# Optimization experiments

Measured on AMD Instinct MI355X. Metric: run time of the kernel, lower is better.

The kernel has to match this reference:

```python
import jax, jax.numpy as jnp
import numpy as np
import math

N_NODES = 50000
N_EDGES = 800000
HIDDEN = 128
NUM_GAUSS = 50
NUM_FILTERS = 128
CUTOFF = 10.0
SHIFT = math.log(2.0)


def setup_inputs() -> dict:
    key = jax.random.key(0)
    ks = jax.random.split(key, 12)
    x = jax.random.normal(ks[0], (N_NODES, HIDDEN), dtype=jnp.float32)
    edge_index = jax.random.randint(ks[1], (2, N_EDGES), 0, N_NODES, dtype=jnp.int64)
    edge_weight = jax.random.uniform(ks[2], (N_EDGES,), dtype=jnp.float32)
    edge_attr = jax.random.normal(ks[3], (N_EDGES, NUM_GAUSS), dtype=jnp.float32)
    # learned parameters (xavier-ish scale)
    def xavier(k, shape):
        fan_in, fan_out = shape[1], shape[0]
        bound = math.sqrt(6.0 / (fan_in + fan_out))
        return jax.random.uniform(k, shape, dtype=jnp.float32, minval=-bound, maxval=bound)
    mlp_w1 = xavier(ks[4], (NUM_FILTERS, NUM_GAUSS))
    mlp_b1 = jnp.zeros((NUM_FILTERS,), jnp.float32)
    mlp_w2 = xavier(ks[5], (NUM_FILTERS, NUM_FILTERS))
    mlp_b2 = jnp.zeros((NUM_FILTERS,), jnp.float32)
    lin1_w = xavier(ks[6], (NUM_FILTERS, HIDDEN))   # no bias
    lin2_w = xavier(ks[7], (HIDDEN, NUM_FILTERS))
    lin2_b = jnp.zeros((HIDDEN,), jnp.float32)
    lin_w = xavier(ks[8], (HIDDEN, HIDDEN))
    lin_b = jnp.zeros((HIDDEN,), jnp.float32)
    return {"x": x, "edge_index": edge_index, "edge_weight": edge_weight,
            "edge_attr": edge_attr, "mlp_w1": mlp_w1, "mlp_b1": mlp_b1,
            "mlp_w2": mlp_w2, "mlp_b2": mlp_b2, "lin1_w": lin1_w,
            "lin2_w": lin2_w, "lin2_b": lin2_b, "lin_w": lin_w, "lin_b": lin_b}


def shifted_softplus(v):
    return jax.nn.softplus(v) - SHIFT


def reference(x, edge_index, edge_weight, edge_attr, mlp_w1, mlp_b1,
              mlp_w2, mlp_b2, lin1_w, lin2_w, lin2_b, lin_w, lin_b):
    src, dst = edge_index[0], edge_index[1]
    # cosine cutoff per edge: [E]
    C = 0.5 * (jnp.cos(edge_weight * (jnp.pi / CUTOFF)) + 1.0)
    # edge filter MLP: [E, num_filters]
    h_e = shifted_softplus(edge_attr @ mlp_w1.T + mlp_b1)
    W = (h_e @ mlp_w2.T + mlp_b2) * C[:, None]
    # node projection, gather-multiply-scatter aggregation
    h = x @ lin1_w.T                       # [N, num_filters]
    msg = h[src] * W                       # [E, num_filters]
    agg = jax.ops.segment_sum(msg, dst, num_segments=N_NODES)  # [N, num_filters]
    h = agg @ lin2_w.T + lin2_b            # [N, hidden]
    h = shifted_softplus(h)
    out = h @ lin_w.T + lin_b              # [N, hidden]
    return out
```

## Files before the change

kernel.cpp:

```cpp
#include <hip/hip_runtime.h>
#include <hip/hip_bf16.h>
#include <math.h>

#define E_NUM 800000
#define NN 50000
#define NG 50
#define NTW (E_NUM / 16)
#define EDGE_BLOCKS 768

typedef __bf16 bf16x8 __attribute__((ext_vector_type(8)));
typedef float f32x4 __attribute__((ext_vector_type(4)));
typedef unsigned short ushortx8 __attribute__((ext_vector_type(8)));

__device__ __forceinline__ unsigned short f2b(float f) {
  union { float f; unsigned u; } v; v.f = f;
  unsigned u = v.u;
  u += 0x7fffu + ((u >> 16) & 1u);
  return (unsigned short)(u >> 16);
}
__device__ __forceinline__ float b2f(unsigned short u) {
  union { unsigned u; float f; } v; v.u = ((unsigned)u) << 16; return v.f;
}
__device__ __forceinline__ float sspf(float v) {
  float e = __builtin_amdgcn_exp2f(-1.4426950408889634f * fabsf(v));
  return fmaxf(v, 0.f) + 0.6931471805599453f * __builtin_amdgcn_logf(fmaf(0.5f, e, 0.5f));
}

__global__ __launch_bounds__(256) void k_hist(const int* __restrict__ ei, int* __restrict__ counts) {
  int e = blockIdx.x * 256 + threadIdx.x;
  if (e < E_NUM) atomicAdd(&counts[ei[E_NUM + e]], 1);
}

__global__ __launch_bounds__(1024) void k_scan(const int* __restrict__ counts,
                                               int* __restrict__ cursor, int* __restrict__ off) {
  __shared__ int tot[1024];
  const int t = threadIdx.x;
  const int C = (NN + 1023) >> 10;
  int lo = t * C, hi = lo + C; if (hi > NN) hi = NN; if (lo > NN) lo = NN;
  int s = 0;
  for (int i = lo; i < hi; ++i) s += counts[i];
  tot[t] = s;
  __syncthreads();
  int mine = s;
  for (int o = 1; o < 1024; o <<= 1) {
    int v = (t >= o) ? tot[t - o] : 0;
    __syncthreads();
    tot[t] += v;
    __syncthreads();
  }
  int run = tot[t] - mine;
  for (int i = lo; i < hi; ++i) { int c = counts[i]; cursor[i] = run; off[i] = run; run += c; }
  if (t == 1023) off[NN] = E_NUM;
}

__global__ __launch_bounds__(256) void k_scatter2(const int* __restrict__ ei,
                                                  int* __restrict__ cursor, int* __restrict__ inv,
                                                  int* __restrict__ srcS) {
  int e = blockIdx.x * 256 + threadIdx.x;
  if (e < E_NUM) {
    int d = ei[E_NUM + e];
    int pos = atomicAdd(&cursor[d], 1);
    inv[e] = pos;
    srcS[pos] = ei[e];
  }
}

__global__ __launch_bounds__(256) void k_mfma_gemm(
    const float* __restrict__ X, const float* __restrict__ Wm,
    const float* __restrict__ bias, float* __restrict__ out, int act, int nrows)
{
  __shared__ __attribute__((aligned(16))) unsigned short s_x[128 * 128];
  __shared__ __attribute__((aligned(16))) unsigned short s_w[128 * 128];
  const int tid = threadIdx.x;
  const int w = tid >> 6, lane = tid & 63, q = lane >> 4, n16 = lane & 15;
  const int base = blockIdx.x * 128;

  for (int c = tid; c < 128 * 16; c += 256) {
    int f = c >> 4, ch = c & 15;
    const float4* wp = (const float4*)(Wm + f * 128 + ch * 8);
    float4 v0 = wp[0], v1 = wp[1];
    ushortx8 v = { f2b(v0.x), f2b(v0.y), f2b(v0.z), f2b(v0.w),
                   f2b(v1.x), f2b(v1.y), f2b(v1.z), f2b(v1.w) };
    *(ushortx8*)&s_w[(f << 7) + ((ch ^ (f & 15)) << 3)] = v;
  }
  for (int c = tid; c < 128 * 16; c += 256) {
    int r = c >> 4, ch = c & 15;
    int n = base + r;
    float4 v0 = {0.f, 0.f, 0.f, 0.f}, v1 = v0;
    if (n < nrows) {
      const float4* xp = (const float4*)(X + (long)n * 128 + ch * 8);
      v0 = xp[0]; v1 = xp[1];
    }
    ushortx8 v = { f2b(v0.x), f2b(v0.y), f2b(v0.z), f2b(v0.w),
                   f2b(v1.x), f2b(v1.y), f2b(v1.z), f2b(v1.w) };
    *(ushortx8*)&s_x[(r << 7) + ((ch ^ (r & 15)) << 3)] = v;
  }
  __syncthreads();

  float bv[8];
#pragma unroll
  for (int t = 0; t < 8; ++t) bv[t] = bias ? bias[t * 16 + n16] : 0.f;

  bf16x8 a[2][4];
#pragma unroll
  for (int g = 0; g < 2; ++g) {
    int r = w * 32 + g * 16 + n16;
#pragma unroll
    for (int ks = 0; ks < 4; ++ks)
      a[g][ks] = *(const bf16x8*)&s_x[(r << 7) + (((ks * 4 + q) ^ (r & 15)) << 3)];
  }
#pragma unroll
  for (int t = 0; t < 8; ++t) {
    int f = t * 16 + n16;
    bf16x8 b[4];
#pragma unroll
    for (int ks = 0; ks < 4; ++ks)
      b[ks] = *(const bf16x8*)&s_w[(f << 7) + (((ks * 4 + q) ^ (f & 15)) << 3)];
#pragma unroll
    for (int g = 0; g < 2; ++g) {
      f32x4 acc = {0.f, 0.f, 0.f, 0.f};
#pragma unroll
      for (int ks = 0; ks < 4; ++ks)
        acc = __builtin_amdgcn_mfma_f32_16x16x32_bf16(a[g][ks], b[ks], acc, 0, 0, 0);
#pragma unroll
      for (int r = 0; r < 4; ++r) {
        int n = base + w * 32 + g * 16 + q * 4 + r;
        if (n < nrows) {
          float v = acc[r] + bv[t];
          if (act) v = sspf(v);
          out[(long)n * 128 + f] = v;
        }
      }
    }
  }
}

__global__ __launch_bounds__(256, 3) void k_edge2(
    const float* __restrict__ attr, const int* __restrict__ ei,
    const float* __restrict__ ew, const float* __restrict__ w1,
    const float* __restrict__ b1, const float* __restrict__ w2,
    const float* __restrict__ b2, const float* __restrict__ h,
    const int* __restrict__ inv, float* __restrict__ agg,
    unsigned short* __restrict__ Wsrt, int mode)
{
  __shared__ __attribute__((aligned(16))) unsigned short s_w2[128 * 128];
  __shared__ __attribute__((aligned(16))) unsigned short s_scr[4 * 16 * 136];

  const int tid  = threadIdx.x;
  const int w    = tid >> 6;
  const int lane = tid & 63;
  const int q    = lane >> 4;
  const int n16  = lane & 15;

  for (int i = tid; i < 128 * 128; i += 256) {
    int f = i >> 7, k = i & 127;
    int pos = (f << 7) + ((((k >> 3) ^ (f & 15)) << 3)) + (k & 7);
    s_w2[pos] = f2b(w2[i]);
  }
  bf16x8 w1A[8], w1B[8];
#pragma unroll
  for (int t = 0; t < 8; ++t) {
    int f = t * 16 + n16;
    const float* row = w1 + f * NG;
    union { ushortx8 u; bf16x8 b; } ua, ub;
#pragma unroll
    for (int j = 0; j < 8; ++j) ua.u[j] = f2b(row[q * 8 + j]);
#pragma unroll
    for (int j = 0; j < 8; ++j) { int k = 32 + q * 8 + j; ub.u[j] = (k < NG) ? f2b(row[k]) : (unsigned short)0; }
    w1A[t] = ua.b; w1B[t] = ub.b;
  }
  float b1v[8], b2v[8];
#pragma unroll
  for (int t = 0; t < 8; ++t) {
    b1v[t] = b1[t * 16 + n16];
    b2v[t] = b2[t * 16 + n16];
  }
  __syncthreads();

  unsigned short* scr = s_scr + w * (16 * 136);
  const int nwaves = EDGE_BLOCKS * 4;
  const int gw = blockIdx.x * 4 + w;

  for (int tile = gw; tile < NTW; tile += nwaves) {
    const int e0 = tile * 16;
    const int er = e0 + n16;
    const float* rp = attr + (long)er * NG;

    float2 p0 = *(const float2*)(rp + q * 8);
    float2 p1 = *(const float2*)(rp + q * 8 + 2);
    float2 p2 = *(const float2*)(rp + q * 8 + 4);
    float2 p3 = *(const float2*)(rp + q * 8 + 6);
    float2 p4 = {0.f, 0.f}, p5 = {0.f, 0.f}, p6 = {0.f, 0.f}, p7 = {0.f, 0.f};
    if (q < 2) {
      const float* rp2 = rp + 32 + q * 8;
      p4 = *(const float2*)(rp2);
      p5 = *(const float2*)(rp2 + 2);
      p6 = *(const float2*)(rp2 + 4);
      p7 = *(const float2*)(rp2 + 6);
    } else if (q == 2) {
      p4 = *(const float2*)(rp + 48);
    }
    union { ushortx8 u; bf16x8 b; } ua, ub;
    ua.u[0] = f2b(p0.x); ua.u[1] = f2b(p0.y); ua.u[2] = f2b(p1.x); ua.u[3] = f2b(p1.y);
    ua.u[4] = f2b(p2.x); ua.u[5] = f2b(p2.y); ua.u[6] = f2b(p3.x); ua.u[7] = f2b(p3.y);
    ub.u[0] = f2b(p4.x); ub.u[1] = f2b(p4.y); ub.u[2] = f2b(p5.x); ub.u[3] = f2b(p5.y);
    ub.u[4] = f2b(p6.x); ub.u[5] = f2b(p6.y); ub.u[6] = f2b(p7.x); ub.u[7] = f2b(p7.y);

#pragma unroll
    for (int t = 0; t < 8; ++t) {
      f32x4 acc = {0.f, 0.f, 0.f, 0.f};
      acc = __builtin_amdgcn_mfma_f32_16x16x32_bf16(ua.b, w1A[t], acc, 0, 0, 0);
      acc = __builtin_amdgcn_mfma_f32_16x16x32_bf16(ub.b, w1B[t], acc, 0, 0, 0);
      int f = t * 16 + n16;
#pragma unroll
      for (int r = 0; r < 4; ++r) {
        int row = q * 4 + r;
        scr[row * 136 + f] = f2b(sspf(acc[r] + b1v[t]));
      }
    }
    __builtin_amdgcn_wave_barrier();

    bf16x8 a2f[4];
#pragma unroll
    for (int ks = 0; ks < 4; ++ks)
      a2f[ks] = *(const bf16x8*)&scr[n16 * 136 + ks * 32 + q * 8];
    __builtin_amdgcn_wave_barrier();

    float cvv[4];
#pragma unroll
    for (int r = 0; r < 4; ++r)
      cvv[r] = 0.5f * (__builtin_amdgcn_cosf(ew[e0 + q * 4 + r] * 0.05f) + 1.f);

    int srcv[4], dstv[4];
    if (mode == 0) {
#pragma unroll
      for (int r = 0; r < 4; ++r) {
        srcv[r] = ei[e0 + q * 4 + r];
        dstv[r] = ei[E_NUM + e0 + q * 4 + r];
      }
    }

#pragma unroll
    for (int t = 0; t < 8; ++t) {
      int f = t * 16 + n16;
      f32x4 acc = {0.f, 0.f, 0.f, 0.f};
#pragma unroll
      for (int ks = 0; ks < 4; ++ks) {
        bf16x8 bb = *(const bf16x8*)&s_w2[(f << 7) + (((ks * 4 + q) ^ (f & 15)) << 3)];
        acc = __builtin_amdgcn_mfma_f32_16x16x32_bf16(a2f[ks], bb, acc, 0, 0, 0);
      }
      if (mode == 1) {
#pragma unroll
        for (int r = 0; r < 4; ++r) {
          int row = q * 4 + r;
          scr[row * 136 + f] = f2b((acc[r] + b2v[t]) * cvv[r]);
        }
      } else {
#pragma unroll
        for (int r = 0; r < 4; ++r) {
          float msg = h[(long)srcv[r] * 128 + f] * (acc[r] + b2v[t]) * cvv[r];
          atomicAdd(&agg[(long)dstv[r] * 128 + f], msg);
        }
      }
    }

    if (mode == 1) {
      __builtin_amdgcn_wave_barrier();
#pragma unroll
      for (int i = 0; i < 4; ++i) {
        int row = i * 4 + q;
        int pos = inv[e0 + row];
        ushortx8 v = *(const ushortx8*)&scr[row * 136 + n16 * 8];
        __builtin_nontemporal_store(v, (ushortx8*)(Wsrt + (long)pos * 128 + n16 * 8));
      }
      __builtin_amdgcn_wave_barrier();
    }
  }
}

__global__ __launch_bounds__(256) void k_e2(
    const unsigned short* __restrict__ Wsrt, const int* __restrict__ srcS,
    const int* __restrict__ off, const float* __restrict__ h, float* __restrict__ agg)
{
  const int wv = threadIdx.x >> 6, lane = threadIdx.x & 63;
  const int n = blockIdx.x * 4 + wv;
  const int j0 = off[n], j1 = off[n + 1];
  float ax = 0.f, ay = 0.f;
  int j = j0;
  for (; j + 4 <= j1; j += 4) {
    int s0 = srcS[j], s1 = srcS[j + 1], s2 = srcS[j + 2], s3 = srcS[j + 3];
    unsigned w0 = __builtin_nontemporal_load((const unsigned*)(Wsrt + (long)(j    ) * 128) + lane);
    unsigned w1_ = __builtin_nontemporal_load((const unsigned*)(Wsrt + (long)(j + 1) * 128) + lane);
    unsigned w2_ = __builtin_nontemporal_load((const unsigned*)(Wsrt + (long)(j + 2) * 128) + lane);
    unsigned w3_ = __builtin_nontemporal_load((const unsigned*)(Wsrt + (long)(j + 3) * 128) + lane);
    float2 h0 = *(const float2*)(h + (long)s0 * 128 + lane * 2);
    float2 h1 = *(const float2*)(h + (long)s1 * 128 + lane * 2);
    float2 h2 = *(const float2*)(h + (long)s2 * 128 + lane * 2);
    float2 h3 = *(const float2*)(h + (long)s3 * 128 + lane * 2);
    ax += h0.x * b2f((unsigned short)(w0 & 0xffffu)) + h1.x * b2f((unsigned short)(w1_ & 0xffffu))
        + h2.x * b2f((unsigned short)(w2_ & 0xffffu)) + h3.x * b2f((unsigned short)(w3_ & 0xffffu));
    ay += h0.y * b2f((unsigned short)(w0 >> 16)) + h1.y * b2f((unsigned short)(w1_ >> 16))
        + h2.y * b2f((unsigned short)(w2_ >> 16)) + h3.y * b2f((unsigned short)(w3_ >> 16));
  }
  for (; j < j1; ++j) {
    int s = srcS[j];
    unsigned wp = __builtin_nontemporal_load((const unsigned*)(Wsrt + (long)j * 128) + lane);
    float2 hp = *(const float2*)(h + (long)s * 128 + lane * 2);
    ax += hp.x * b2f((unsigned short)(wp & 0xffffu));
    ay += hp.y * b2f((unsigned short)(wp >> 16));
  }
  float2 o; o.x = ax; o.y = ay;
  *(float2*)(agg + (long)n * 128 + lane * 2) = o;
}

extern "C" void kernel_launch(void* const* d_in, const int* in_sizes, int n_in,
                              void* d_out, int out_size, void* d_ws, size_t ws_size,
                              hipStream_t stream) {
  const float* x     = (const float*)d_in[0];
  const int*   ei    = (const int*)  d_in[1];
  const float* ew    = (const float*)d_in[2];
  const float* attr  = (const float*)d_in[3];
  const float* w1    = (const float*)d_in[4];
  const float* b1    = (const float*)d_in[5];
  const float* w2    = (const float*)d_in[6];
  const float* b2    = (const float*)d_in[7];
  const float* lin1w = (const float*)d_in[8];
  const float* lin2w = (const float*)d_in[9];
  const float* lin2b = (const float*)d_in[10];
  const float* linw  = (const float*)d_in[11];
  const float* linb  = (const float*)d_in[12];
  float* out = (float*)d_out;

  char* base = (char*)d_ws;
  float* agg    = (float*)base;
  float* h      = agg + (size_t)NN * 128;
  int*   counts = (int*)(h + (size_t)NN * 128);
  int*   cursor = counts + NN;
  int*   off    = cursor + NN;
  int*   inv    = off + NN + 1;
  int*   srcS   = inv + E_NUM;
  size_t head   = (size_t)((char*)(srcS + E_NUM) - base);
  size_t woff   = (head + 255) & ~(size_t)255;
  unsigned short* Wsrt = (unsigned short*)(base + woff);
  size_t need = woff + (size_t)E_NUM * 128 * sizeof(unsigned short);
  const int mode = (ws_size >= need) ? 1 : 0;

  const int gemm_grid = (NN + 127) / 128;
  if (mode == 1) {
    (void)hipMemsetAsync(counts, 0, (size_t)NN * sizeof(int), stream);
    k_hist<<<(E_NUM + 255) / 256, 256, 0, stream>>>(ei, counts);
    k_scan<<<1, 1024, 0, stream>>>(counts, cursor, off);
    k_scatter2<<<(E_NUM + 255) / 256, 256, 0, stream>>>(ei, cursor, inv, srcS);
    k_edge2<<<EDGE_BLOCKS, 256, 0, stream>>>(attr, ei, ew, w1, b1, w2, b2, h, inv, agg, Wsrt, 1);
    k_mfma_gemm<<<gemm_grid, 256, 0, stream>>>(x, lin1w, nullptr, h, 0, NN);
    k_e2<<<NN / 4, 256, 0, stream>>>(Wsrt, srcS, off, h, agg);
  } else {
    (void)hipMemsetAsync(agg, 0, (size_t)NN * 128 * sizeof(float), stream);
    k_mfma_gemm<<<gemm_grid, 256, 0, stream>>>(x, lin1w, nullptr, h, 0, NN);
    k_edge2<<<EDGE_BLOCKS, 256, 0, stream>>>(attr, ei, ew, w1, b1, w2, b2, h, inv, agg, Wsrt, 0);
  }
  k_mfma_gemm<<<gemm_grid, 256, 0, stream>>>(agg, lin2w, lin2b, h, 1, NN);
  k_mfma_gemm<<<gemm_grid, 256, 0, stream>>>(h, linw, linb, out, 0, NN);
}
```

Baseline: 672.4 us.

## Fuse edge filter with sorted-segment aggregation and fuse the two output GEMMs

The edge kernel now processes edges in dst-sorted order. It gathers attr and edge_weight through a permutation, then reduces each 16-edge tile's messages per destination in registers. Interior runs are plain stores and boundary runs use atomics, so the bf16 W buffer and the separate k_e2 aggregation pass are gone. The last two node GEMMs are fused into one kernel that keeps the intermediate in shared memory. This removes the large write and read of the per-edge filter matrix, but adds scattered attr gathers, atomics at tile boundaries and a full agg memset.

```diff
diff --git a/kernel.cpp b/kernel.cpp
--- a/kernel.cpp
+++ b/kernel.cpp
@@ -13,10 +13,7 @@
 typedef unsigned short ushortx8 __attribute__((ext_vector_type(8)));
 
 __device__ __forceinline__ unsigned short f2b(float f) {
-  union { float f; unsigned u; } v; v.f = f;
-  unsigned u = v.u;
-  u += 0x7fffu + ((u >> 16) & 1u);
-  return (unsigned short)(u >> 16);
+  union { __bf16 h; unsigned short u; } v; v.h = (__bf16)f; return v.u;
 }
 __device__ __forceinline__ float b2f(unsigned short u) {
   union { unsigned u; float f; } v; v.u = ((unsigned)u) << 16; return v.f;
@@ -54,14 +51,16 @@
 }
 
 __global__ __launch_bounds__(256) void k_scatter2(const int* __restrict__ ei,
-                                                  int* __restrict__ cursor, int* __restrict__ inv,
-                                                  int* __restrict__ srcS) {
+                                                  int* __restrict__ cursor,
+                                                  int* __restrict__ srcS, int* __restrict__ dstS,
+                                                  int* __restrict__ eS) {
   int e = blockIdx.x * 256 + threadIdx.x;
   if (e < E_NUM) {
     int d = ei[E_NUM + e];
     int pos = atomicAdd(&cursor[d], 1);
-    inv[e] = pos;
     srcS[pos] = ei[e];
+    dstS[pos] = d;
+    eS[pos] = e;
   }
 }
 
@@ -135,13 +134,129 @@
   }
 }
 
-__global__ __launch_bounds__(256, 3) void k_edge2(
+__global__ __launch_bounds__(256, 2) void k_gemm23(
+    const float* __restrict__ A, const float* __restrict__ W2,
+    const float* __restrict__ B2, const float* __restrict__ W3,
+    const float* __restrict__ B3, float* __restrict__ out, int nrows)
+{
+  __shared__ __attribute__((aligned(16))) unsigned short s_x[128 * 128];
+  __shared__ __attribute__((aligned(16))) unsigned short s_w[128 * 128];
+  const int tid = threadIdx.x;
+  const int w = tid >> 6, lane = tid & 63, q = lane >> 4, n16 = lane & 15;
+  const int base = blockIdx.x * 128;
+
+  for (int c = tid; c < 128 * 16; c += 256) {
+    int f = c >> 4, ch = c & 15;
+    const float4* wp = (const float4*)(W2 + f * 128 + ch * 8);
+    float4 v0 = wp[0], v1 = wp[1];
+    ushortx8 v = { f2b(v0.x), f2b(v0.y), f2b(v0.z), f2b(v0.w),
+                   f2b(v1.x), f2b(v1.y), f2b(v1.z), f2b(v1.w) };
+    *(ushortx8*)&s_w[(f << 7) + ((ch ^ (f & 15)) << 3)] = v;
+  }
+  for (int c = tid; c < 128 * 16; c += 256) {
+    int r = c >> 4, ch = c & 15;
+    int n = base + r;
+    float4 v0 = {0.f, 0.f, 0.f, 0.f}, v1 = v0;
+    if (n < nrows) {
+      const float4* xp = (const float4*)(A + (long)n * 128 + ch * 8);
+      v0 = xp[0]; v1 = xp[1];
+    }
+    ushortx8 v = { f2b(v0.x), f2b(v0.y), f2b(v0.z), f2b(v0.w),
+                   f2b(v1.x), f2b(v1.y), f2b(v1.z), f2b(v1.w) };
+    *(ushortx8*)&s_x[(r << 7) + ((ch ^ (r & 15)) << 3)] = v;
+  }
+  __syncthreads();
+
+  float b2v[8], b3v[8];
+#pragma unroll
+  for (int t = 0; t < 8; ++t) { b2v[t] = B2[t * 16 + n16]; b3v[t] = B3[t * 16 + n16]; }
+
+  bf16x8 a[2][4];
+#pragma unroll
+  for (int g = 0; g < 2; ++g) {
+    int r = w * 32 + g * 16 + n16;
+#pragma unroll
+    for (int ks = 0; ks < 4; ++ks)
+      a[g][ks] = *(const bf16x8*)&s_x[(r << 7) + (((ks * 4 + q) ^ (r & 15)) << 3)];
+  }
+  float acc1[8][2][4];
+#pragma unroll
+  for (int t = 0; t < 8; ++t) {
+    int f = t * 16 + n16;
+    bf16x8 b[4];
+#pragma unroll
+    for (int ks = 0; ks < 4; ++ks)
+      b[ks] = *(const bf16x8*)&s_w[(f << 7) + (((ks * 4 + q) ^ (f & 15)) << 3)];
+#pragma unroll
+    for (int g = 0; g < 2; ++g) {
+      f32x4 acc = {0.f, 0.f, 0.f, 0.f};
+#pragma unroll
+      for (int ks = 0; ks < 4; ++ks)
+        acc = __builtin_amdgcn_mfma_f32_16x16x32_bf16(a[g][ks], b[ks], acc, 0, 0, 0);
+#pragma unroll
+      for (int r = 0; r < 4; ++r) acc1[t][g][r] = acc[r];
+    }
+  }
+  __syncthreads();
+
+#pragma unroll
+  for (int t = 0; t < 8; ++t) {
+    int f = t * 16 + n16;
+#pragma unroll
+    for (int g = 0; g < 2; ++g)
+#pragma unroll
+      for (int r = 0; r < 4; ++r) {
+        int row = w * 32 + g * 16 + q * 4 + r;
+        s_x[(row << 7) + (((f >> 3) ^ (row & 15)) << 3) + (f & 7)] =
+            f2b(sspf(acc1[t][g][r] + b2v[t]));
+      }
+  }
+  for (int c = tid; c < 128 * 16; c += 256) {
+    int f = c >> 4, ch = c & 15;
+    const float4* wp = (const float4*)(W3 + f * 128 + ch * 8);
+    float4 v0 = wp[0], v1 = wp[1];
+    ushortx8 v = { f2b(v0.x), f2b(v0.y), f2b(v0.z), f2b(v0.w),
+                   f2b(v1.x), f2b(v1.y), f2b(v1.z), f2b(v1.w) };
+    *(ushortx8*)&s_w[(f << 7) + ((ch ^ (f & 15)) << 3)] = v;
+  }
+  __syncthreads();
+
+#pragma unroll
+  for (int g = 0; g < 2; ++g) {
+    int r = w * 32 + g * 16 + n16;
+#pragma unroll
+    for (int ks = 0; ks < 4; ++ks)
+      a[g][ks] = *(const bf16x8*)&s_x[(r << 7) + (((ks * 4 + q) ^ (r & 15)) << 3)];
+  }
+#pragma unroll
+  for (int t = 0; t < 8; ++t) {
+    int f = t * 16 + n16;
+    bf16x8 b[4];
+#pragma unroll
+    for (int ks = 0; ks < 4; ++ks)
+      b[ks] = *(const bf16x8*)&s_w[(f << 7) + (((ks * 4 + q) ^ (f & 15)) << 3)];
+#pragma unroll
+    for (int g = 0; g < 2; ++g) {
+      f32x4 acc = {0.f, 0.f, 0.f, 0.f};
+#pragma unroll
+      for (int ks = 0; ks < 4; ++ks)
+        acc = __builtin_amdgcn_mfma_f32_16x16x32_bf16(a[g][ks], b[ks], acc, 0, 0, 0);
+#pragma unroll
+      for (int r = 0; r < 4; ++r) {
+        int n = base + w * 32 + g * 16 + q * 4 + r;
+        if (n < nrows) out[(long)n * 128 + f] = acc[r] + b3v[t];
+      }
+    }
+  }
+}
+
+__global__ __launch_bounds__(256, 3) void k_edge_agg(
     const float* __restrict__ attr, const int* __restrict__ ei,
     const float* __restrict__ ew, const float* __restrict__ w1,
     const float* __restrict__ b1, const float* __restrict__ w2,
     const float* __restrict__ b2, const float* __restrict__ h,
-    const int* __restrict__ inv, float* __restrict__ agg,
-    unsigned short* __restrict__ Wsrt, int mode)
+    const int* __restrict__ srcS, const int* __restrict__ dstS,
+    const int* __restrict__ eS, float* __restrict__ agg, int mode)
 {
   __shared__ __attribute__((aligned(16))) unsigned short s_w2[128 * 128];
   __shared__ __attribute__((aligned(16))) unsigned short s_scr[4 * 16 * 136];
@@ -183,8 +298,8 @@
 
   for (int tile = gw; tile < NTW; tile += nwaves) {
     const int e0 = tile * 16;
-    const int er = e0 + n16;
-    const float* rp = attr + (long)er * NG;
+    const int eA = (mode == 1) ? eS[e0 + n16] : (e0 + n16);
+    const float* rp = attr + (long)eA * NG;
 
     float2 p0 = *(const float2*)(rp + q * 8);
     float2 p1 = *(const float2*)(rp + q * 8 + 2);
@@ -228,8 +343,10 @@
 
     float cvv[4];
 #pragma unroll
-    for (int r = 0; r < 4; ++r)
-      cvv[r] = 0.5f * (__builtin_amdgcn_cosf(ew[e0 + q * 4 + r] * 0.05f) + 1.f);
+    for (int r = 0; r < 4; ++r) {
+      int ee = (mode == 1) ? eS[e0 + q * 4 + r] : (e0 + q * 4 + r);
+      cvv[r] = 0.5f * (__builtin_amdgcn_cosf(ew[ee] * 0.05f) + 1.f);
+    }
 
     int srcv[4], dstv[4];
     if (mode == 0) {
@@ -266,51 +383,41 @@
 
     if (mode == 1) {
       __builtin_amdgcn_wave_barrier();
-#pragma unroll
-      for (int i = 0; i < 4; ++i) {
-        int row = i * 4 + q;
-        int pos = inv[e0 + row];
-        ushortx8 v = *(const ushortx8*)&scr[row * 136 + n16 * 8];
-        __builtin_nontemporal_store(v, (ushortx8*)(Wsrt + (long)pos * 128 + n16 * 8));
+      int dcur = -1, rowstart = 0;
+      float ax = 0.f, ay = 0.f;
+#pragma unroll
+      for (int hf = 0; hf < 2; ++hf) {
+        int dv[8]; float2 hv[8];
+#pragma unroll
+        for (int i = 0; i < 8; ++i) {
+          int pos = e0 + hf * 8 + i;
+          dv[i] = __builtin_amdgcn_readfirstlane(dstS[pos]);
+          int sv = __builtin_amdgcn_readfirstlane(srcS[pos]);
+          hv[i] = *(const float2*)(h + (long)sv * 128 + (lane << 1));
+        }
+#pragma unroll
+        for (int i = 0; i < 8; ++i) {
+          int row = hf * 8 + i;
+          if (dv[i] != dcur) {
+            if (dcur >= 0) {
+              float* ap = agg + (long)dcur * 128 + (lane << 1);
+              if (rowstart == 0) { atomicAdd(ap, ax); atomicAdd(ap + 1, ay); }
+              else { float2 o; o.x = ax; o.y = ay; *(float2*)ap = o; }
+            }
+            dcur = dv[i]; ax = 0.f; ay = 0.f; rowstart = row;
+          }
+          unsigned wp = *(const unsigned*)&scr[row * 136 + (lane << 1)];
+          ax = fmaf(hv[i].x, b2f((unsigned short)(wp & 0xffffu)), ax);
+          ay = fmaf(hv[i].y, b2f((unsigned short)(wp >> 16)), ay);
+        }
+      }
+      {
+        float* ap = agg + (long)dcur * 128 + (lane << 1);
+        atomicAdd(ap, ax); atomicAdd(ap + 1, ay);
       }
       __builtin_amdgcn_wave_barrier();
     }
   }
-}
-
-__global__ __launch_bounds__(256) void k_e2(
-    const unsigned short* __restrict__ Wsrt, const int* __restrict__ srcS,
-    const int* __restrict__ off, const float* __restrict__ h, float* __restrict__ agg)
-{
-  const int wv = threadIdx.x >> 6, lane = threadIdx.x & 63;
-  const int n = blockIdx.x * 4 + wv;
-  const int j0 = off[n], j1 = off[n + 1];
-  float ax = 0.f, ay = 0.f;
-  int j = j0;
-  for (; j + 4 <= j1; j += 4) {
-    int s0 = srcS[j], s1 = srcS[j + 1], s2 = srcS[j + 2], s3 = srcS[j + 3];
-    unsigned w0 = __builtin_nontemporal_load((const unsigned*)(Wsrt + (long)(j    ) * 128) + lane);
-    unsigned w1_ = __builtin_nontemporal_load((const unsigned*)(Wsrt + (long)(j + 1) * 128) + lane);
-    unsigned w2_ = __builtin_nontemporal_load((const unsigned*)(Wsrt + (long)(j + 2) * 128) + lane);
-    unsigned w3_ = __builtin_nontemporal_load((const unsigned*)(Wsrt + (long)(j + 3) * 128) + lane);
-    float2 h0 = *(const float2*)(h + (long)s0 * 128 + lane * 2);
-    float2 h1 = *(const float2*)(h + (long)s1 * 128 + lane * 2);
-    float2 h2 = *(const float2*)(h + (long)s2 * 128 + lane * 2);
-    float2 h3 = *(const float2*)(h + (long)s3 * 128 + lane * 2);
-    ax += h0.x * b2f((unsigned short)(w0 & 0xffffu)) + h1.x * b2f((unsigned short)(w1_ & 0xffffu))
-        + h2.x * b2f((unsigned short)(w2_ & 0xffffu)) + h3.x * b2f((unsigned short)(w3_ & 0xffffu));
-    ay += h0.y * b2f((unsigned short)(w0 >> 16)) + h1.y * b2f((unsigned short)(w1_ >> 16))
-        + h2.y * b2f((unsigned short)(w2_ >> 16)) + h3.y * b2f((unsigned short)(w3_ >> 16));
-  }
-  for (; j < j1; ++j) {
-    int s = srcS[j];
-    unsigned wp = __builtin_nontemporal_load((const unsigned*)(Wsrt + (long)j * 128) + lane);
-    float2 hp = *(const float2*)(h + (long)s * 128 + lane * 2);
-    ax += hp.x * b2f((unsigned short)(wp & 0xffffu));
-    ay += hp.y * b2f((unsigned short)(wp >> 16));
-  }
-  float2 o; o.x = ax; o.y = ay;
-  *(float2*)(agg + (long)n * 128 + lane * 2) = o;
 }
 
 extern "C" void kernel_launch(void* const* d_in, const int* in_sizes, int n_in,
@@ -337,28 +444,22 @@
   int*   counts = (int*)(h + (size_t)NN * 128);
   int*   cursor = counts + NN;
   int*   off    = cursor + NN;
-  int*   inv    = off + NN + 1;
-  int*   srcS   = inv + E_NUM;
-  size_t head   = (size_t)((char*)(srcS + E_NUM) - base);
-  size_t woff   = (head + 255) & ~(size_t)255;
-  unsigned short* Wsrt = (unsigned short*)(base + woff);
-  size_t need = woff + (size_t)E_NUM * 128 * sizeof(unsigned short);
+  int*   srcS   = off + NN + 1;
+  int*   dstS   = srcS + E_NUM;
+  int*   eS     = dstS + E_NUM;
+  size_t need   = (size_t)((char*)(eS + E_NUM) - base);
   const int mode = (ws_size >= need) ? 1 : 0;
 
   const int gemm_grid = (NN + 127) / 128;
+  (void)hipMemsetAsync(agg, 0, (size_t)NN * 128 * sizeof(float), stream);
   if (mode == 1) {
     (void)hipMemsetAsync(counts, 0, (size_t)NN * sizeof(int), stream);
     k_hist<<<(E_NUM + 255) / 256, 256, 0, stream>>>(ei, counts);
     k_scan<<<1, 1024, 0, stream>>>(counts, cursor, off);
-    k_scatter2<<<(E_NUM + 255) / 256, 256, 0, stream>>>(ei, cursor, inv, srcS);
-    k_edge2<<<EDGE_BLOCKS, 256, 0, stream>>>(attr, ei, ew, w1, b1, w2, b2, h, inv, agg, Wsrt, 1);
-    k_mfma_gemm<<<gemm_grid, 256, 0, stream>>>(x, lin1w, nullptr, h, 0, NN);
-    k_e2<<<NN / 4, 256, 0, stream>>>(Wsrt, srcS, off, h, agg);
-  } else {
-    (void)hipMemsetAsync(agg, 0, (size_t)NN * 128 * sizeof(float), stream);
-    k_mfma_gemm<<<gemm_grid, 256, 0, stream>>>(x, lin1w, nullptr, h, 0, NN);
-    k_edge2<<<EDGE_BLOCKS, 256, 0, stream>>>(attr, ei, ew, w1, b1, w2, b2, h, inv, agg, Wsrt, 0);
-  }
-  k_mfma_gemm<<<gemm_grid, 256, 0, stream>>>(agg, lin2w, lin2b, h, 1, NN);
-  k_mfma_gemm<<<gemm_grid, 256, 0, stream>>>(h, linw, linb, out, 0, NN);
-}
+    k_scatter2<<<(E_NUM + 255) / 256, 256, 0, stream>>>(ei, cursor, srcS, dstS, eS);
+  }
+  k_mfma_gemm<<<gemm_grid, 256, 0, stream>>>(x, lin1w, nullptr, h, 0, NN);
+  k_edge_agg<<<EDGE_BLOCKS, 256, 0, stream>>>(attr, ei, ew, w1, b1, w2, b2, h,
+                                              srcS, dstS, eS, agg, mode);
+  k_gemm23<<<gemm_grid, 256, 0, stream>>>(agg, lin2w, lin2b, linw, linb, out, NN);
+}
```

Result: faster. 640.6 us (-4.7%).
